# Performance work log

Hardware: AMD Instinct MI355X
Metric: run time of the kernel (lower is better)

The kernel has to match this reference:

```python
import jax, jax.numpy as jnp
import numpy as np

D_MODEL = 1024
N_HEADS = 16
D_K = D_MODEL // N_HEADS
D_FF = 4096
EPS = 1e-5


def _layer_norm(x, gamma, beta):
    mu = jnp.mean(x, axis=-1, keepdims=True)
    var = jnp.var(x, axis=-1, keepdims=True)
    return (x - mu) * jax.lax.rsqrt(var + EPS) * gamma + beta


def setup_inputs() -> dict:
    key = jax.random.key(0)
    ks = jax.random.split(key, 16)
    s = 1.0 / np.sqrt(D_MODEL)
    sf = 1.0 / np.sqrt(D_FF)
    return {
        "x": jax.random.normal(ks[0], (2, 2048, D_MODEL), dtype=jnp.float32),
        "Wq": jax.random.uniform(ks[1], (D_MODEL, D_MODEL), minval=-s, maxval=s),
        "bq": jax.random.uniform(ks[2], (D_MODEL,), minval=-s, maxval=s),
        "Wk": jax.random.uniform(ks[3], (D_MODEL, D_MODEL), minval=-s, maxval=s),
        "bk": jax.random.uniform(ks[4], (D_MODEL,), minval=-s, maxval=s),
        "Wv": jax.random.uniform(ks[5], (D_MODEL, D_MODEL), minval=-s, maxval=s),
        "bv": jax.random.uniform(ks[6], (D_MODEL,), minval=-s, maxval=s),
        "Wo": jax.random.uniform(ks[7], (D_MODEL, D_MODEL), minval=-s, maxval=s),
        "bo": jax.random.uniform(ks[8], (D_MODEL,), minval=-s, maxval=s),
        "W1": jax.random.uniform(ks[9], (D_MODEL, D_FF), minval=-s, maxval=s),
        "b1": jax.random.uniform(ks[10], (D_FF,), minval=-s, maxval=s),
        "W2": jax.random.uniform(ks[11], (D_FF, D_MODEL), minval=-sf, maxval=sf),
        "b2": jax.random.uniform(ks[12], (D_MODEL,), minval=-sf, maxval=sf),
        "g1": jnp.ones((D_MODEL,)),
        "be1": jnp.zeros((D_MODEL,)),
        "g2": jnp.ones((D_MODEL,)),
        "be2": jnp.zeros((D_MODEL,)),
    }


def reference(x, Wq, bq, Wk, bk, Wv, bv, Wo, bo, W1, b1, W2, b2, g1, be1, g2, be2):
    B, S, _ = x.shape

    def heads(y):  # (B,S,D) -> (B,H,S,dk)
        return y.reshape(B, S, N_HEADS, D_K).transpose(0, 2, 1, 3)

    q = heads(x @ Wq + bq)
    k = heads(x @ Wk + bk)
    v = heads(x @ Wv + bv)

    scores = jnp.einsum("bhqd,bhkd->bhqk", q, k) / np.sqrt(D_K)
    attn = jax.nn.softmax(scores, axis=-1)
    out = jnp.einsum("bhqk,bhkd->bhqd", attn, v)
    out = out.transpose(0, 2, 1, 3).reshape(B, S, D_MODEL)
    attn_out = out @ Wo + bo

    resid_mid = _layer_norm(x + attn_out, g1, be1)
    ff = jnp.maximum(resid_mid @ W1 + b1, 0.0) @ W2 + b2
    return _layer_norm(resid_mid + ff, g2, be2)
```

## Files before the change

kernel.cpp:

```cpp
#include <hip/hip_runtime.h>

#define DM   1024
#define DFF  4096
#define NH   16
#define DKH  64
#define SEQ  2048
#define BATCH 2
#define ROWS (BATCH*SEQ)
#define QKS  2048

typedef __bf16 bf16x8 __attribute__((ext_vector_type(8)));
typedef float  f32x4  __attribute__((ext_vector_type(4)));

__device__ __forceinline__ unsigned short f2b(float f) {
    unsigned int u = __builtin_bit_cast(unsigned int, f);
    u += 0x7fffu + ((u >> 16) & 1u);
    return (unsigned short)(u >> 16);
}
__device__ __forceinline__ float b2f(unsigned short u) {
    return __builtin_bit_cast(float, (unsigned int)u << 16);
}
__device__ __forceinline__ float exp2_raw(float x) {
    float r;
    asm("v_exp_f32 %0, %1" : "=v"(r) : "v"(x));
    return r;
}

__device__ __forceinline__ void gl_lds16(const unsigned short* g, unsigned short* l) {
    __builtin_amdgcn_global_load_lds(
        (const __attribute__((address_space(1))) unsigned int*)(const void*)g,
        (__attribute__((address_space(3))) unsigned int*)(void*)l, 16, 0, 0);
}

__global__ __launch_bounds__(256) void k_f32_to_bf16(const float* __restrict__ in,
                                                     unsigned short* __restrict__ out, int n4) {
    int i = blockIdx.x * 256 + threadIdx.x;
    if (i < n4) {
        float4 v = ((const float4*)in)[i];
        ushort4 u;
        u.x = f2b(v.x); u.y = f2b(v.y); u.z = f2b(v.z); u.w = f2b(v.w);
        ((ushort4*)out)[i] = u;
    }
}

__global__ __launch_bounds__(256) void k_transpose_bf16(const float* __restrict__ W,
                                                        unsigned short* __restrict__ WT,
                                                        int R, int C) {
    __shared__ float t[32][33];
    int c0 = blockIdx.x * 32, r0 = blockIdx.y * 32;
    int tx = threadIdx.x, ty = threadIdx.y;
#pragma unroll
    for (int i = 0; i < 4; i++) {
        int r = ty + i * 8;
        t[r][tx] = W[(size_t)(r0 + r) * C + c0 + tx];
    }
    __syncthreads();
#pragma unroll
    for (int i = 0; i < 4; i++) {
        int r = ty + i * 8;
        WT[(size_t)(c0 + r) * R + r0 + tx] = f2b(t[tx][r]);
    }
}

template<int WM, int WN, bool OUTF32, bool RELU, bool BIASROW, bool VPERM, bool SCALE2, bool SPLITK>
__global__ __launch_bounds__(256) void k_gemm_bt(const unsigned short* __restrict__ A,
                                                 const unsigned short* __restrict__ BT,
                                                 const float* __restrict__ bias,
                                                 const float* __restrict__ bias2,
                                                 int bsplit, float sc2,
                                                 void* __restrict__ Cout,
                                                 int M, int N, int K) {
    constexpr int BM = 2 * WM, BN = 2 * WN;
    constexpr int MT = WM / 16, NT = WN / 16;
    constexpr int IA = BM / 32, IB = BN / 32;
    __shared__ unsigned short As[BM][64] __attribute__((aligned(16)));
    __shared__ unsigned short Bs[BN][64] __attribute__((aligned(16)));
    int tid = threadIdx.x;
    int w = tid >> 6, l = tid & 63;
    int wr = w >> 1, wc = w & 1;
    int l15 = l & 15, lg = l >> 4;

    int bid = blockIdx.y * gridDim.x + blockIdx.x;
    int nwg = gridDim.x * gridDim.y;
    int swz = (bid & 7) * (nwg >> 3) + (bid >> 3);
    int m0 = (swz / gridDim.x) * BM, n0 = (swz % gridDim.x) * BN;

    int kb_ = SPLITK ? (int)blockIdx.z * (K >> 1) : 0;
    int Keff = SPLITK ? (K >> 1) : K;

    int lr8 = l >> 3;
    int gsrc = (l & 7) ^ lr8;
    const unsigned short* Abase = A  + (size_t)(m0 + w * (BM / 4) + lr8) * K + kb_ + gsrc * 8;
    const unsigned short* Bbase = BT + (size_t)(n0 + w * (BN / 4) + lr8) * K + kb_ + gsrc * 8;

    f32x4 acc[MT][NT] = {};

    int nk = Keff >> 6;
    for (int kt = 0; kt < nk; ++kt) {
        __syncthreads();
#pragma unroll
        for (int it = 0; it < IA; ++it)
            gl_lds16(Abase + (size_t)(it * 8) * K + kt * 64, &As[w * (BM / 4) + it * 8][0]);
#pragma unroll
        for (int it = 0; it < IB; ++it)
            gl_lds16(Bbase + (size_t)(it * 8) * K + kt * 64, &Bs[w * (BN / 4) + it * 8][0]);
        __syncthreads();
#pragma unroll
        for (int ks = 0; ks < 2; ++ks) {
            int glog = ks * 4 + lg;
            bf16x8 af[MT], bfr[NT];
#pragma unroll
            for (int mt = 0; mt < MT; ++mt) {
                int row = wr * WM + mt * 16 + l15;
                af[mt] = *(const bf16x8*)&As[row][(glog ^ (row & 7)) << 3];
            }
#pragma unroll
            for (int nt = 0; nt < NT; ++nt) {
                int row = wc * WN + nt * 16 + l15;
                bfr[nt] = *(const bf16x8*)&Bs[row][(glog ^ (row & 7)) << 3];
            }
#pragma unroll
            for (int mt = 0; mt < MT; ++mt)
#pragma unroll
                for (int nt = 0; nt < NT; ++nt)
                    acc[mt][nt] = __builtin_amdgcn_mfma_f32_16x16x32_bf16(af[mt], bfr[nt], acc[mt][nt], 0, 0, 0);
        }
    }
    float* CoutF = (float*)Cout + (SPLITK ? (size_t)blockIdx.z * M * N : 0);
    float browv[MT][4];
    if (BIASROW) {
#pragma unroll
        for (int mt = 0; mt < MT; ++mt)
#pragma unroll
            for (int r = 0; r < 4; ++r)
                browv[mt][r] = bias[m0 + wr * WM + mt * 16 + lg * 4 + r];
    }
#pragma unroll
    for (int nt = 0; nt < NT; ++nt) {
        int colo = VPERM ? (32 * (nt >> 1) + 4 * (nt & 1) + 8 * (l15 >> 2) + (l15 & 3))
                         : (nt * 16 + l15);
        int col = n0 + wc * WN + colo;
        float bv = BIASROW ? 0.f : (col < bsplit ? bias[col] : bias2[col - bsplit]);
        if (SPLITK && blockIdx.z != 0) bv = 0.f;
#pragma unroll
        for (int mt = 0; mt < MT; ++mt) {
#pragma unroll
            for (int r = 0; r < 4; ++r) {
                int row = m0 + wr * WM + mt * 16 + lg * 4 + r;
                float v = acc[mt][nt][r] + (BIASROW ? browv[mt][r] : bv);
                if (SCALE2 && col >= bsplit) v *= sc2;
                if (RELU) v = fmaxf(v, 0.f);
                if (OUTF32) CoutF[(size_t)row * N + col] = v;
                else        ((unsigned short*)Cout)[(size_t)row * N + col] = f2b(v);
            }
        }
    }
}

__global__ __launch_bounds__(512) void k_attn(const unsigned short* __restrict__ Q,
                                              const unsigned short* __restrict__ Kb,
                                              const unsigned short* __restrict__ VT,
                                              unsigned short* __restrict__ O) {
    __shared__ unsigned short ksA[64][64] __attribute__((aligned(16)));
    __shared__ unsigned short vsA[64][64] __attribute__((aligned(16)));
    __shared__ unsigned short ksB[64][64] __attribute__((aligned(16)));
    __shared__ unsigned short vsB[64][64] __attribute__((aligned(16)));

    int tid = threadIdx.x;
    int w = tid >> 6, l = tid & 63;
    int l15 = l & 15, lg = l >> 4;

    int bid = blockIdx.y * gridDim.x + blockIdx.x;
    int bh = (bid & 7) * 4 + ((bid >> 3) & 3);
    int qt = bid >> 5;
    int b = bh >> 4, h = bh & 15;
    int row0 = qt * 128;

    const unsigned short* qg  = Q  + (size_t)b * SEQ * QKS + h * DKH;
    const unsigned short* kg  = Kb + (size_t)b * SEQ * QKS + h * DKH;
    const unsigned short* vtg = VT + (size_t)(h * DKH) * ROWS + (size_t)b * SEQ;

    int lr8 = l >> 3;
    int gsrc = (l & 7) ^ lr8;

    const unsigned short* kp0 = kg  + (size_t)(w * 8 + lr8) * QKS + gsrc * 8;
    const unsigned short* vp0 = vtg + (size_t)(w * 8 + lr8) * ROWS + gsrc * 8;

    gl_lds16(kp0, &ksA[w * 8][0]);
    gl_lds16(vp0, &vsA[w * 8][0]);
    kp0 += (size_t)64 * QKS; vp0 += 64;

    bf16x8 aq[2];
    {
        int qrow = row0 + w * 16 + l15;
        aq[0] = *(const bf16x8*)(qg + (size_t)qrow * QKS + lg * 8);
        aq[1] = *(const bf16x8*)(qg + (size_t)qrow * QKS + (4 + lg) * 8);
    }

    int dsoff[2][4];
#pragma unroll
    for (int ksi = 0; ksi < 2; ksi++)
#pragma unroll
        for (int nt = 0; nt < 4; nt++) {
            int row = nt * 16 + l15;
            int glog = ksi * 4 + lg;
            dsoff[ksi][nt] = row * 128 + ((glog ^ (row & 7)) << 4);
        }

    union { bf16x8 v; unsigned int u[4]; } ones;
#pragma unroll
    for (int i = 0; i < 4; i++) ones.u[i] = 0x3f803f80u;

    f32x4 o[4] = {};
    f32x4 osum = {};

    __syncthreads();

    auto body = [&](unsigned short (&kbuf)[64][64], unsigned short (&vbuf)[64][64],
                    unsigned short (&knext)[64][64], unsigned short (&vnext)[64][64],
                    bool doStage) {
        if (doStage) {
            gl_lds16(kp0, &knext[w * 8][0]);
            gl_lds16(vp0, &vnext[w * 8][0]);
            kp0 += (size_t)64 * QKS; vp0 += 64;
        }

        f32x4 s[4] = {};
        __builtin_amdgcn_s_setprio(1);
#pragma unroll
        for (int ksi = 0; ksi < 2; ksi++)
#pragma unroll
            for (int nt = 0; nt < 4; nt++) {
                bf16x8 bk = *(const bf16x8*)((const char*)&kbuf[0][0] + dsoff[ksi][nt]);
                s[nt] = __builtin_amdgcn_mfma_f32_16x16x32_bf16(bk, aq[ksi], s[nt], 0, 0, 0);
            }
        __builtin_amdgcn_s_setprio(0);

        union { bf16x8 v; unsigned int u[4]; } A0, A1;
#pragma unroll
        for (int nt = 0; nt < 4; nt++)
#pragma unroll
            for (int w2 = 0; w2 < 2; w2++) {
                float e0 = exp2_raw(s[nt][2 * w2]);
                float e1 = exp2_raw(s[nt][2 * w2 + 1]);
                unsigned int pk;
                asm("v_cvt_pk_bf16_f32 %0, %1, %2" : "=v"(pk) : "v"(e0), "v"(e1));
                if (nt < 2) A0.u[(nt & 1) * 2 + w2] = pk;
                else        A1.u[(nt & 1) * 2 + w2] = pk;
            }

        __builtin_amdgcn_s_setprio(1);
        osum = __builtin_amdgcn_mfma_f32_16x16x32_bf16(A0.v, ones.v, osum, 0, 0, 0);
        osum = __builtin_amdgcn_mfma_f32_16x16x32_bf16(A1.v, ones.v, osum, 0, 0, 0);
#pragma unroll
        for (int ksi = 0; ksi < 2; ksi++)
#pragma unroll
            for (int nt = 0; nt < 4; nt++) {
                bf16x8 bv = *(const bf16x8*)((const char*)&vbuf[0][0] + dsoff[ksi][nt]);
                o[nt] = __builtin_amdgcn_mfma_f32_16x16x32_bf16(ksi == 0 ? A0.v : A1.v, bv, o[nt], 0, 0, 0);
            }
        __builtin_amdgcn_s_setprio(0);

        __syncthreads();
    };

    for (int kt2 = 0; kt2 < 16; ++kt2) {
        body(ksA, vsA, ksB, vsB, true);
        body(ksB, vsB, ksA, vsA, kt2 < 15);
    }

    float rinv[4];
#pragma unroll
    for (int r = 0; r < 4; r++) rinv[r] = 1.f / osum[r];

    unsigned short* og = O + (size_t)b * SEQ * DM + h * DKH;
#pragma unroll
    for (int nt = 0; nt < 4; nt++) {
        int d = nt * 16 + l15;
#pragma unroll
        for (int r = 0; r < 4; r++) {
            int srow_ = row0 + w * 16 + lg * 4 + r;
            og[(size_t)srow_ * DM + d] = f2b(o[nt][r] * rinv[r]);
        }
    }
}

template<bool WB16, bool ADD3>
__global__ __launch_bounds__(256) void k_add_ln(const float* __restrict__ a,
                                                const float* __restrict__ b,
                                                const float* __restrict__ c,
                                                const float* __restrict__ gamma,
                                                const float* __restrict__ beta,
                                                float* __restrict__ outf,
                                                unsigned short* __restrict__ outb) {
    __shared__ float red[8];
    int row = blockIdx.x, tid = threadIdx.x;
    float4 va = ((const float4*)(a + (size_t)row * DM))[tid];
    float4 vb = ((const float4*)(b + (size_t)row * DM))[tid];
    float4 v;
    v.x = va.x + vb.x; v.y = va.y + vb.y; v.z = va.z + vb.z; v.w = va.w + vb.w;
    if (ADD3) {
        float4 vc = ((const float4*)(c + (size_t)row * DM))[tid];
        v.x += vc.x; v.y += vc.y; v.z += vc.z; v.w += vc.w;
    }
    float s = v.x + v.y + v.z + v.w;
    float q = v.x * v.x + v.y * v.y + v.z * v.z + v.w * v.w;
#pragma unroll
    for (int m = 1; m < 64; m <<= 1) { s += __shfl_xor(s, m); q += __shfl_xor(q, m); }
    if ((tid & 63) == 0) { red[tid >> 6] = s; red[4 + (tid >> 6)] = q; }
    __syncthreads();
    float tot  = red[0] + red[1] + red[2] + red[3];
    float totq = red[4] + red[5] + red[6] + red[7];
    float mu = tot * (1.f / DM);
    float var = totq * (1.f / DM) - mu * mu;
    float rs = rsqrtf(var + 1e-5f);
    float4 g  = ((const float4*)gamma)[tid];
    float4 be = ((const float4*)beta)[tid];
    float4 y;
    y.x = (v.x - mu) * rs * g.x + be.x;
    y.y = (v.y - mu) * rs * g.y + be.y;
    y.z = (v.z - mu) * rs * g.z + be.z;
    y.w = (v.w - mu) * rs * g.w + be.w;
    ((float4*)(outf + (size_t)row * DM))[tid] = y;
    if (WB16) {
        ushort4 u;
        u.x = f2b(y.x); u.y = f2b(y.y); u.z = f2b(y.z); u.w = f2b(y.w);
        ((ushort4*)(outb + (size_t)row * DM))[tid] = u;
    }
}

extern "C" void kernel_launch(void* const* d_in, const int* in_sizes, int n_in,
                              void* d_out, int out_size, void* d_ws, size_t ws_size,
                              hipStream_t stream) {
    const float* x   = (const float*)d_in[0];
    const float* Wq  = (const float*)d_in[1];
    const float* bq  = (const float*)d_in[2];
    const float* Wk  = (const float*)d_in[3];
    const float* bk  = (const float*)d_in[4];
    const float* Wv  = (const float*)d_in[5];
    const float* bv  = (const float*)d_in[6];
    const float* Wo  = (const float*)d_in[7];
    const float* bo  = (const float*)d_in[8];
    const float* W1  = (const float*)d_in[9];
    const float* b1  = (const float*)d_in[10];
    const float* W2  = (const float*)d_in[11];
    const float* b2  = (const float*)d_in[12];
    const float* g1  = (const float*)d_in[13];
    const float* be1 = (const float*)d_in[14];
    const float* g2  = (const float*)d_in[15];
    const float* be2 = (const float*)d_in[16];

    char* ws = (char*)d_ws;
    const size_t MB = 1u << 20;
    unsigned short* xb    = (unsigned short*)(ws + 0);
    unsigned short* WqkT  = (unsigned short*)(ws + 8 * MB);
    unsigned short* WvT   = (unsigned short*)(ws + 12 * MB);
    unsigned short* WoT   = (unsigned short*)(ws + 14 * MB);
    unsigned short* W1T   = (unsigned short*)(ws + 16 * MB);
    unsigned short* W2T   = (unsigned short*)(ws + 24 * MB);
    unsigned short* qkb   = (unsigned short*)(ws + 32 * MB);
    unsigned short* vT    = (unsigned short*)(ws + 48 * MB);
    float*          ff2p  = (float*)(ws + 32 * MB);
    float*          scrf  = (float*)(ws + 56 * MB);
    float*          resid = (float*)(ws + 72 * MB);
    unsigned short* residb= (unsigned short*)(ws + 88 * MB);
    unsigned short* h1    = (unsigned short*)(ws + 96 * MB);

    dim3 blk(256);
    dim3 tb(32, 8);
    const int BIG = 1 << 30;
    const float SC = 0.125f * 1.44269504f;

    k_f32_to_bf16<<<(ROWS * DM / 4 + 255) / 256, blk, 0, stream>>>(x, xb, ROWS * DM / 4);
    k_transpose_bf16<<<dim3(DM / 32, DM / 32), tb, 0, stream>>>(Wq, WqkT, DM, DM);
    k_transpose_bf16<<<dim3(DM / 32, DM / 32), tb, 0, stream>>>(Wk, WqkT + (size_t)DM * DM, DM, DM);
    k_transpose_bf16<<<dim3(DM / 32, DM / 32), tb, 0, stream>>>(Wv, WvT, DM, DM);
    k_transpose_bf16<<<dim3(DM / 32, DM / 32), tb, 0, stream>>>(Wo, WoT, DM, DM);
    k_transpose_bf16<<<dim3(DFF / 32, DM / 32), tb, 0, stream>>>(W1, W1T, DM, DFF);
    k_transpose_bf16<<<dim3(DM / 32, DFF / 32), tb, 0, stream>>>(W2, W2T, DFF, DM);

    k_gemm_bt<32, 64, false, false, false, false, true, false><<<dim3(QKS / 128, ROWS / 64), blk, 0, stream>>>(
        xb, WqkT, bq, bk, DM, SC, qkb, ROWS, QKS, DM);
    k_gemm_bt<32, 64, false, false, true, true, false, false><<<dim3(ROWS / 128, DM / 64), blk, 0, stream>>>(
        WvT, xb, bv, bv, BIG, 1.f, vT, DM, ROWS, DM);

    k_attn<<<dim3(SEQ / 128, BATCH * NH), dim3(512), 0, stream>>>(qkb, qkb + DM, vT, xb);

    k_gemm_bt<32, 64, true, false, false, false, false, false><<<dim3(DM / 128, ROWS / 64), blk, 0, stream>>>(
        xb, WoT, bo, bo, BIG, 1.f, scrf, ROWS, DM, DM);
    k_add_ln<true, false><<<ROWS, blk, 0, stream>>>(x, scrf, nullptr, g1, be1, resid, residb);

    k_gemm_bt<64, 64, false, true, false, false, false, false><<<dim3(DFF / 128, ROWS / 128), blk, 0, stream>>>(
        residb, W1T, b1, b1, BIG, 1.f, h1, ROWS, DFF, DM);
    k_gemm_bt<32, 64, true, false, false, false, false, true><<<dim3(DM / 128, ROWS / 64, 2), blk, 0, stream>>>(
        h1, W2T, b2, b2, BIG, 1.f, ff2p, ROWS, DM, DFF);
    k_add_ln<false, true><<<ROWS, blk, 0, stream>>>(resid, ff2p, ff2p + (size_t)ROWS * DM, g2, be2, (float*)d_out, nullptr);
}
```

Baseline: 240.5 us.

## Merge prep kernels, split-K the Wo GEMM, add XCD-aware 2D tile mapping for W1

Replaces the seven cast and transpose launches with one k_prep launch that uses blockIdx.z to pick the tensor, which cuts launch overhead and lets the small transposes overlap. The Wo projection GEMM now uses split-K=2 so it launches twice as many workgroups, and the first add+LayerNorm sums the two partial outputs. The W1 GEMM gets a SUPER2D block mapping that gives each XCD a contiguous 2D region of tiles, aiming at better L2 reuse. In exchange, split-K writes and reads an extra fp32 partial buffer, and k_prep launches many idle blocks that exit early.

```diff
diff --git a/kernel.cpp b/kernel.cpp
--- a/kernel.cpp
+++ b/kernel.cpp
@@ -32,23 +32,41 @@
         (__attribute__((address_space(3))) unsigned int*)(void*)l, 16, 0, 0);
 }
 
-__global__ __launch_bounds__(256) void k_f32_to_bf16(const float* __restrict__ in,
-                                                     unsigned short* __restrict__ out, int n4) {
-    int i = blockIdx.x * 256 + threadIdx.x;
-    if (i < n4) {
-        float4 v = ((const float4*)in)[i];
+__global__ __launch_bounds__(256) void k_prep(const float* __restrict__ x,
+                                              const float* __restrict__ Wq,
+                                              const float* __restrict__ Wk,
+                                              const float* __restrict__ Wv,
+                                              const float* __restrict__ Wo,
+                                              const float* __restrict__ W1,
+                                              const float* __restrict__ W2,
+                                              unsigned short* __restrict__ xb,
+                                              unsigned short* __restrict__ WqkT,
+                                              unsigned short* __restrict__ WvT,
+                                              unsigned short* __restrict__ WoT,
+                                              unsigned short* __restrict__ W1T,
+                                              unsigned short* __restrict__ W2T) {
+    int z = blockIdx.z;
+    int bid = blockIdx.y * gridDim.x + blockIdx.x;
+    int tx = threadIdx.x, ty = threadIdx.y;
+    if (z == 6) {
+        int i = bid * 256 + ty * 32 + tx;
+        float4 v = ((const float4*)x)[i];
         ushort4 u;
         u.x = f2b(v.x); u.y = f2b(v.y); u.z = f2b(v.z); u.w = f2b(v.w);
-        ((ushort4*)out)[i] = u;
-    }
-}
-
-__global__ __launch_bounds__(256) void k_transpose_bf16(const float* __restrict__ W,
-                                                        unsigned short* __restrict__ WT,
-                                                        int R, int C) {
+        ((ushort4*)xb)[i] = u;
+        return;
+    }
+    const float* W; unsigned short* WT; int R, C;
+    if      (z == 0) { W = Wq; WT = WqkT;                     R = DM;  C = DM;  }
+    else if (z == 1) { W = Wk; WT = WqkT + (size_t)DM * DM;   R = DM;  C = DM;  }
+    else if (z == 2) { W = Wv; WT = WvT;                      R = DM;  C = DM;  }
+    else if (z == 3) { W = Wo; WT = WoT;                      R = DM;  C = DM;  }
+    else if (z == 4) { W = W1; WT = W1T;                      R = DM;  C = DFF; }
+    else             { W = W2; WT = W2T;                      R = DFF; C = DM;  }
+    int ct = C / 32;
+    if (bid >= (R / 32) * ct) return;
+    int c0 = (bid % ct) * 32, r0 = (bid / ct) * 32;
     __shared__ float t[32][33];
-    int c0 = blockIdx.x * 32, r0 = blockIdx.y * 32;
-    int tx = threadIdx.x, ty = threadIdx.y;
 #pragma unroll
     for (int i = 0; i < 4; i++) {
         int r = ty + i * 8;
@@ -62,7 +80,7 @@
     }
 }
 
-template<int WM, int WN, bool OUTF32, bool RELU, bool BIASROW, bool VPERM, bool SCALE2, bool SPLITK>
+template<int WM, int WN, bool OUTF32, bool RELU, bool BIASROW, bool VPERM, bool SCALE2, bool SPLITK, bool SUPER2D>
 __global__ __launch_bounds__(256) void k_gemm_bt(const unsigned short* __restrict__ A,
                                                  const unsigned short* __restrict__ BT,
                                                  const float* __restrict__ bias,
@@ -82,8 +100,17 @@
 
     int bid = blockIdx.y * gridDim.x + blockIdx.x;
     int nwg = gridDim.x * gridDim.y;
-    int swz = (bid & 7) * (nwg >> 3) + (bid >> 3);
-    int m0 = (swz / gridDim.x) * BM, n0 = (swz % gridDim.x) * BN;
+    int m0, n0;
+    if (SUPER2D) {
+        int xcd = bid & 7, q = bid >> 3;
+        int RM = gridDim.y >> 1, RN = gridDim.x >> 2;
+        int mI = (xcd >> 2) * RM + (q % RM);
+        int nI = (xcd & 3) * RN + (q / RM);
+        m0 = mI * BM; n0 = nI * BN;
+    } else {
+        int swz = (bid & 7) * (nwg >> 3) + (bid >> 3);
+        m0 = (swz / gridDim.x) * BM; n0 = (swz % gridDim.x) * BN;
+    }
 
     int kb_ = SPLITK ? (int)blockIdx.z * (K >> 1) : 0;
     int Keff = SPLITK ? (K >> 1) : K;
@@ -360,39 +387,32 @@
     unsigned short* W2T   = (unsigned short*)(ws + 24 * MB);
     unsigned short* qkb   = (unsigned short*)(ws + 32 * MB);
     unsigned short* vT    = (unsigned short*)(ws + 48 * MB);
-    float*          ff2p  = (float*)(ws + 32 * MB);
-    float*          scrf  = (float*)(ws + 56 * MB);
+    float*          prt   = (float*)(ws + 32 * MB);
     float*          resid = (float*)(ws + 72 * MB);
     unsigned short* residb= (unsigned short*)(ws + 88 * MB);
     unsigned short* h1    = (unsigned short*)(ws + 96 * MB);
 
     dim3 blk(256);
-    dim3 tb(32, 8);
     const int BIG = 1 << 30;
     const float SC = 0.125f * 1.44269504f;
 
-    k_f32_to_bf16<<<(ROWS * DM / 4 + 255) / 256, blk, 0, stream>>>(x, xb, ROWS * DM / 4);
-    k_transpose_bf16<<<dim3(DM / 32, DM / 32), tb, 0, stream>>>(Wq, WqkT, DM, DM);
-    k_transpose_bf16<<<dim3(DM / 32, DM / 32), tb, 0, stream>>>(Wk, WqkT + (size_t)DM * DM, DM, DM);
-    k_transpose_bf16<<<dim3(DM / 32, DM / 32), tb, 0, stream>>>(Wv, WvT, DM, DM);
-    k_transpose_bf16<<<dim3(DM / 32, DM / 32), tb, 0, stream>>>(Wo, WoT, DM, DM);
-    k_transpose_bf16<<<dim3(DFF / 32, DM / 32), tb, 0, stream>>>(W1, W1T, DM, DFF);
-    k_transpose_bf16<<<dim3(DM / 32, DFF / 32), tb, 0, stream>>>(W2, W2T, DFF, DM);
-
-    k_gemm_bt<32, 64, false, false, false, false, true, false><<<dim3(QKS / 128, ROWS / 64), blk, 0, stream>>>(
+    k_prep<<<dim3(128, 32, 7), dim3(32, 8), 0, stream>>>(x, Wq, Wk, Wv, Wo, W1, W2,
+                                                         xb, WqkT, WvT, WoT, W1T, W2T);
+
+    k_gemm_bt<32, 64, false, false, false, false, true, false, false><<<dim3(QKS / 128, ROWS / 64), blk, 0, stream>>>(
         xb, WqkT, bq, bk, DM, SC, qkb, ROWS, QKS, DM);
-    k_gemm_bt<32, 64, false, false, true, true, false, false><<<dim3(ROWS / 128, DM / 64), blk, 0, stream>>>(
+    k_gemm_bt<32, 64, false, false, true, true, false, false, false><<<dim3(ROWS / 128, DM / 64), blk, 0, stream>>>(
         WvT, xb, bv, bv, BIG, 1.f, vT, DM, ROWS, DM);
 
     k_attn<<<dim3(SEQ / 128, BATCH * NH), dim3(512), 0, stream>>>(qkb, qkb + DM, vT, xb);
 
-    k_gemm_bt<32, 64, true, false, false, false, false, false><<<dim3(DM / 128, ROWS / 64), blk, 0, stream>>>(
-        xb, WoT, bo, bo, BIG, 1.f, scrf, ROWS, DM, DM);
-    k_add_ln<true, false><<<ROWS, blk, 0, stream>>>(x, scrf, nullptr, g1, be1, resid, residb);
-
-    k_gemm_bt<64, 64, false, true, false, false, false, false><<<dim3(DFF / 128, ROWS / 128), blk, 0, stream>>>(
+    k_gemm_bt<32, 64, true, false, false, false, false, true, false><<<dim3(DM / 128, ROWS / 64, 2), blk, 0, stream>>>(
+        xb, WoT, bo, bo, BIG, 1.f, prt, ROWS, DM, DM);
+    k_add_ln<true, true><<<ROWS, blk, 0, stream>>>(x, prt, prt + (size_t)ROWS * DM, g1, be1, resid, residb);
+
+    k_gemm_bt<64, 64, false, true, false, false, false, false, true><<<dim3(DFF / 128, ROWS / 128), blk, 0, stream>>>(
         residb, W1T, b1, b1, BIG, 1.f, h1, ROWS, DFF, DM);
-    k_gemm_bt<32, 64, true, false, false, false, false, true><<<dim3(DM / 128, ROWS / 64, 2), blk, 0, stream>>>(
-        h1, W2T, b2, b2, BIG, 1.f, ff2p, ROWS, DM, DFF);
-    k_add_ln<false, true><<<ROWS, blk, 0, stream>>>(resid, ff2p, ff2p + (size_t)ROWS * DM, g2, be2, (float*)d_out, nullptr);
-}
+    k_gemm_bt<32, 64, true, false, false, false, false, true, false><<<dim3(DM / 128, ROWS / 64, 2), blk, 0, stream>>>(
+        h1, W2T, b2, b2, BIG, 1.f, prt, ROWS, DM, DFF);
+    k_add_ln<false, true><<<ROWS, blk, 0, stream>>>(resid, prt, prt + (size_t)ROWS * DM, g2, be2, (float*)d_out, nullptr);
+}
```

Measured after the change: 230.8 us. 1.04x faster.
